# Optimization experiments

Measured on AMD Instinct MI355X. Metric: run time of the kernel, lower is better.

Reference implementation:

```python
import jax
import jax.numpy as jnp
import numpy as np
from jax import lax

DELTA = float(np.exp(-2.0))  # rule-creation density threshold


def codebook_lamb(x):
    """Online growing RBF prototype codebook (ALMMo-style) for one layer.

    x: [N, M]. Returns lamb: [N] normalized density of each sample at its
    assigned rule. Faithful (corrected) semantics of Layer.__call__:
      - SEN = squared L2 norm per sample (over feature dim)
      - global mean / mean squared norm over the batch
      - sequential per-sample: if max RBF density over existing rules < exp(-2),
        append a new rule (prototype=c=x, SENc=||x||^2, support=1);
        else update rule_star. Note the source's `support[rule_star] = +1`
        assigns 1, so the running mean update degenerates to c[rule_star]=x,
        SENc[rule_star]=||x||^2 -- replicated here.
      - distances use the (never-updated) prototypes; bandwidth stau uses c.
    """
    N, M = x.shape
    SENx = jnp.sum(x * x, axis=-1)                      # [N]
    gmean = jnp.mean(x, axis=0)                         # [M]
    base = jnp.mean(SENx) - jnp.sum(gmean * gmean)      # SENgmean - SEN(gmean)
    R = N                                               # worst case: one rule/sample

    protos0 = jnp.zeros((R, M), x.dtype)
    pn20 = jnp.zeros((R,), x.dtype)                     # ||proto_r||^2 (carried)
    c0 = jnp.zeros((R, M), x.dtype)
    cn20 = jnp.zeros((R,), x.dtype)                     # ||c_r||^2 (carried)
    SENc0 = jnp.zeros((R,), x.dtype)
    count0 = jnp.int32(0)

    ridx = jnp.arange(R)

    def step(carry, inp):
        protos, pn2, c, cn2, SENc, count = carry
        xi, sxi = inp                                   # [M], scalar
        valid = ridx < count
        stau = (base + SENc - cn2) * 0.5                # [R]
        dist = sxi + pn2 - 2.0 * (protos @ xi)          # [R] ||xi - proto_r||^2
        dens = jnp.where(valid, jnp.exp(-dist / stau), -jnp.inf)
        idx = jnp.argmax(dens)
        vmax = dens[idx]
        new = (count == 0) | (vmax < DELTA)
        slot = jnp.where(new, count, idx)
        # both branches set c/SENc at slot to xi/sxi (support resets to 1)
        c = c.at[slot].set(xi)
        cn2 = cn2.at[slot].set(sxi)
        SENc = SENc.at[slot].set(sxi)
        # only a new rule writes a prototype (OOB scatter when count==R is dropped)
        protos = protos.at[count].set(jnp.where(new, xi, protos[count]))
        pn2 = pn2.at[count].set(jnp.where(new, sxi, pn2[count]))
        count = count + new.astype(count.dtype)
        return (protos, pn2, c, cn2, SENc, count), slot

    (protos, pn2, c, cn2, SENc, count), rules = lax.scan(
        step, (protos0, pn20, c0, cn20, SENc0, count0), (x, SENx)
    )

    # final densities of all samples under all (valid) rules: [R, N]
    stau = (base + SENc - cn2) * 0.5                    # [R]
    dist = SENx[None, :] + pn2[:, None] - 2.0 * (protos @ x.T)
    dens = jnp.where((ridx < count)[:, None], jnp.exp(-dist / stau[:, None]), 0.0)
    dens_xn = dens[rules, jnp.arange(N)]                # density at assigned rule
    lamb = dens_xn / jnp.sum(dens, axis=0)              # normalize over rules
    return lamb


def setup_inputs() -> dict:
    key = jax.random.key(0)
    k = jax.random.split(key, 5)
    N, D_IN, D_H, D_OUT = 2048, 2048, 2048, 1024
    s0 = 1.0 / np.sqrt(D_IN)
    s1 = 1.0 / np.sqrt(D_H)
    return {
        "x": jax.random.normal(k[0], (N, D_IN), jnp.float32),
        "W0": jax.random.normal(k[1], (D_H, D_IN), jnp.float32) * s0,
        "b0": jax.random.normal(k[2], (D_H,), jnp.float32) * s0,
        "W1": jax.random.normal(k[3], (D_OUT, D_H), jnp.float32) * s1,
        "b1": jax.random.normal(k[4], (D_OUT,), jnp.float32) * s1,
    }


def reference(x, W0, b0, W1, b1):
    lambs = []
    h = x
    for W, b in ((W0, b0), (W1, b1)):
        lambs.append(codebook_lamb(h))          # per-layer codebook on layer input
        h = jax.nn.sigmoid(h @ W.T + b)         # torch.nn.Linear + sigmoid
    return h, jnp.stack(lambs)                  # ([N, d_out], [n_layers, N])
```

## Files before the change

kernel.cpp:

```cpp
#include <hip/hip_runtime.h>
#include <cstdint>
#include <cstddef>


#define DELTA_F 0.13533528323661270f
#define MBYTE (1u << 20)

typedef __bf16 bf16;
typedef bf16 bf16x8 __attribute__((ext_vector_type(8)));
typedef bf16 bf16x4 __attribute__((ext_vector_type(4)));
typedef float f32x4 __attribute__((ext_vector_type(4)));

typedef __attribute__((address_space(1))) void as1_void;
typedef __attribute__((address_space(3))) void as3_void;

__device__ __forceinline__ void gload16(const bf16* g, bf16* l) {
  __builtin_amdgcn_global_load_lds((as1_void*)g, (as3_void*)l, 16, 0, 0);
}

__device__ __forceinline__ float wave_reduce(float s) {
  for (int o = 32; o > 0; o >>= 1) s += __shfl_down(s, o, 64);
  return s;
}

template <bool IS_L0>
__global__ __launch_bounds__(512, 4) void gemm_fused(
    const bf16* __restrict__ A, float* __restrict__ Dens,
    bf16* __restrict__ Hb, float* __restrict__ Fo,
    const float* __restrict__ bias, const float* __restrict__ SENin,
    const float* __restrict__ ninv_p, float* __restrict__ S,
    int* __restrict__ e, float* __restrict__ SENhOut,
    float* __restrict__ colsumH, float* __restrict__ diagD,
    int* __restrict__ cnt, float* __restrict__ scalOut,
    float* __restrict__ lambOut, int nblocks) {
  __shared__ __align__(16) char smem[32768];
  __shared__ int s_last;
  const int tid = threadIdx.x;
  const int wave = tid >> 6, lane = tid & 63;
  const int quad = lane >> 4, l16 = lane & 15;
  const int kg = wave & 1, wm = (wave >> 1) & 1, wn = (wave >> 2) & 1;
  const int m0 = blockIdx.y * 128, n0 = blockIdx.x * 128;
  const int waveM = wm * 64, waveN = wn * 64;
  const bool isGram = (n0 < 2048);
  const int sr8 = lane >> 3, slot = lane & 7;
  const int gk = (slot ^ sr8) * 8;
  const bf16* aSrc = A + (size_t)(m0 + wave * 16 + sr8) * 2048 + gk;
  const bf16* bSrc = A + (size_t)(n0 + wave * 16 + sr8) * 2048 + gk;
  char* const aDst = smem + wave * 2048;
  char* const bDst = smem + 16384 + wave * 2048;
  const int swz = ((kg * 4 + quad) ^ (l16 & 7)) * 16;
  const int aOff = (waveM + l16) * 128 + swz;
  const int bOff = 16384 + (waveN + l16) * 128 + swz;

  f32x4 acc[4][4] = {};
  for (int k0 = 0; k0 < 2048; k0 += 64) {
    gload16(aSrc + k0, (bf16*)aDst);
    gload16(aSrc + 8 * 2048 + k0, (bf16*)(aDst + 1024));
    gload16(bSrc + k0, (bf16*)bDst);
    gload16(bSrc + 8 * 2048 + k0, (bf16*)(bDst + 1024));
    __syncthreads();
    bf16x8 af[4], bfr[4];
#pragma unroll
    for (int i = 0; i < 4; ++i) af[i] = *(const bf16x8*)(smem + aOff + i * 2048);
#pragma unroll
    for (int j = 0; j < 4; ++j) bfr[j] = *(const bf16x8*)(smem + bOff + j * 2048);
#pragma unroll
    for (int i = 0; i < 4; ++i)
#pragma unroll
      for (int j = 0; j < 4; ++j)
        acc[i][j] = __builtin_amdgcn_mfma_f32_16x16x32_bf16(af[i], bfr[j], acc[i][j], 0, 0, 0);
    __syncthreads();
  }

  const float ninv = ninv_p[0];
  float colp[4] = {0.f, 0.f, 0.f, 0.f};
  char* const ex = smem + (wn * 2 + wm) * 8192;
#pragma unroll
  for (int round = 0; round < 2; ++round) {
    __syncthreads();
    if (kg == 1) {
#pragma unroll
      for (int ii = 0; ii < 2; ++ii)
#pragma unroll
        for (int j = 0; j < 4; ++j)
          *(f32x4*)(ex + (ii * 4 + j) * 1024 + lane * 16) = acc[round * 2 + ii][j];
    }
    __syncthreads();
    if (kg == 0) {
#pragma unroll
      for (int ii = 0; ii < 2; ++ii) {
        const int i = round * 2 + ii;
        const int rbase = m0 + waveM + i * 16 + quad * 4;
        if (isGram) {
          const f32x4 si4 = *(const f32x4*)(SENin + rbase);
          float rp[4] = {0.f, 0.f, 0.f, 0.f};
          int er = 0;
#pragma unroll
          for (int j = 0; j < 4; ++j) {
            f32x4 v = acc[i][j] + *(const f32x4*)(ex + (ii * 4 + j) * 1024 + lane * 16);
            const int col = n0 + waveN + j * 16 + l16;
            const float sj = SENin[col];
#pragma unroll
            for (int r = 0; r < 4; ++r) {
              const float dens = __expf((si4[r] + sj - 2.0f * v[r]) * ninv);
              Dens[(size_t)(rbase + r) * 2048 + col] = dens;
              rp[r] += dens;
              if (col < rbase + r && dens >= DELTA_F) er |= (1 << r);
              if (col == rbase + r) atomicExch(diagD + col, dens);
            }
          }
#pragma unroll
          for (int r = 0; r < 4; ++r) {
            float rv = rp[r];
            rv += __shfl_xor(rv, 1, 64); rv += __shfl_xor(rv, 2, 64);
            rv += __shfl_xor(rv, 4, 64); rv += __shfl_xor(rv, 8, 64);
            if (l16 == 0) atomicAdd(S + rbase + r, rv);
          }
          er |= __shfl_xor(er, 1, 64); er |= __shfl_xor(er, 2, 64);
          er |= __shfl_xor(er, 4, 64); er |= __shfl_xor(er, 8, 64);
          if (l16 == 0 && er) {
#pragma unroll
            for (int r = 0; r < 4; ++r)
              if ((er >> r) & 1) atomicOr(e + rbase + r, 1);
          }
        } else {
          float rn[4] = {0.f, 0.f, 0.f, 0.f};
#pragma unroll
          for (int j = 0; j < 4; ++j) {
            f32x4 v = acc[i][j] + *(const f32x4*)(ex + (ii * 4 + j) * 1024 + lane * 16);
            const int c2 = n0 - 2048 + waveN + j * 16 + l16;
            const float bv = bias[c2];
#pragma unroll
            for (int r = 0; r < 4; ++r) {
              const float hv = 1.0f / (1.0f + __expf(-(v[r] + bv)));
              if (IS_L0) {
                Hb[(size_t)(rbase + r) * 2048 + c2] = (bf16)hv;
                rn[r] += hv * hv;
                colp[j] += hv;
              } else {
                Fo[(size_t)(rbase + r) * 1024 + c2] = hv;
              }
            }
          }
          if (IS_L0) {
#pragma unroll
            for (int r = 0; r < 4; ++r) {
              float rv = rn[r];
              rv += __shfl_xor(rv, 1, 64); rv += __shfl_xor(rv, 2, 64);
              rv += __shfl_xor(rv, 4, 64); rv += __shfl_xor(rv, 8, 64);
              if (l16 == 0) atomicAdd(SENhOut + rbase + r, rv);
            }
          }
        }
      }
    }
  }
  if (IS_L0 && !isGram && kg == 0) {
#pragma unroll
    for (int j = 0; j < 4; ++j) {
      float cv = colp[j];
      cv += __shfl_xor(cv, 16, 64);
      cv += __shfl_xor(cv, 32, 64);
      if (lane < 16) atomicAdd(colsumH + (n0 - 2048 + waveN + j * 16 + lane), cv);
    }
  }

  __syncthreads();
  if (tid == 0) s_last = (atomicAdd(cnt, 1) == nblocks - 1);
  __syncthreads();
  if (!s_last) return;

  char* s_flag = smem;
  short* s_as = (short*)(smem + 2048);
  short* s_list = (short*)(smem + 6144);
  short* s_re = (short*)(smem + 10240);
  int* scan_ = (int*)(smem + 14336);
  float* rbest = (float*)(smem + 16384);
  int* rbj = (int*)(smem + 18432);
  float* r1 = (float*)(smem + 20480);
  float* r2 = (float*)(smem + 22528);
  int* sT = (int*)(smem + 24576);
  int* sReN = (int*)(smem + 24580);

  if (IS_L0) {
    float ssen = 0.f, sg2 = 0.f;
    for (int i = tid; i < 2048; i += 512) ssen += atomicAdd(SENhOut + i, 0.f);
    for (int c = tid; c < 2048; c += 512) {
      const float gm = atomicAdd(colsumH + c, 0.f) * (1.f / 2048.f);
      sg2 += gm * gm;
    }
    r1[tid] = ssen; r2[tid] = sg2;
    __syncthreads();
    for (int s = 256; s; s >>= 1) {
      if (tid < s) { r1[tid] += r1[tid + s]; r2[tid] += r2[tid + s]; }
      __syncthreads();
    }
    if (tid == 0) {
      const float stau = 0.5f * (r1[0] * (1.f / 2048.f) - r2[0]);
      scalOut[4] = stau;
      scalOut[5] = -1.f / stau;
    }
    __syncthreads();
  }

  int cntl = 0;
#pragma unroll
  for (int k = 0; k < 4; ++k) {
    const int i = tid * 4 + k;
    const int ei = atomicOr(e + i, 0);
    s_flag[i] = (ei == 0);
    if (ei == 0) s_as[i] = (short)i;
    cntl += (ei != 0);
  }
  scan_[tid] = cntl;
  if (tid == 0) sReN[0] = 0;
  __syncthreads();
  for (int off = 1; off < 512; off <<= 1) {
    const int v = scan_[tid];
    const int add = (tid >= off) ? scan_[tid - off] : 0;
    __syncthreads();
    scan_[tid] = v + add;
    __syncthreads();
  }
  int pos = scan_[tid] - cntl;
#pragma unroll
  for (int k = 0; k < 4; ++k) {
    const int i = tid * 4 + k;
    if (!s_flag[i]) s_list[pos++] = (short)i;
  }
  if (tid == 511) sT[0] = scan_[511];
  __syncthreads();
  const int T = sT[0];
  if (T > 0) __threadfence();
  for (int t = 0; t < T; ++t) {
    const int i = s_list[t];
    const float* di = Dens + (size_t)i * 2048;
    float best = -1.0f;
    int bestj = 0x7fffffff;
    for (int j = tid; j < i; j += 512) {
      if (s_flag[j]) {
        const float d = di[j];
        if (d > best || (d == best && j < bestj)) { best = d; bestj = j; }
      }
    }
    rbest[tid] = best; rbj[tid] = bestj;
    __syncthreads();
    if (tid == 0) {
      float b = -1.0f;
      int bj = 0x7fffffff;
      for (int k = 0; k < 512; ++k)
        if (rbest[k] > b || (rbest[k] == b && rbj[k] < bj)) { b = rbest[k]; bj = rbj[k]; }
      if (b < DELTA_F) { s_flag[i] = 1; s_as[i] = (short)i; }
      else { s_as[i] = (short)bj; s_re[sReN[0]++] = (short)i; }
    }
    __syncthreads();
  }
  const int reN = sReN[0];

#pragma unroll
  for (int k = 0; k < 4; ++k) {
    const int n = k * 512 + tid;
    const int aa = s_as[n];
    const float num = (aa == n) ? atomicAdd(diagD + n, 0.f)
                                : Dens[(size_t)n * 2048 + aa];
    float denom = atomicAdd(S + n, 0.f);
    for (int t = 0; t < reN; ++t) denom -= Dens[(size_t)n * 2048 + s_re[t]];
    lambOut[n] = num / denom;
  }
}

__global__ void f2b_all(const float* __restrict__ x, const float* __restrict__ W0,
                        const float* __restrict__ W1, bf16* __restrict__ xb,
                        bf16* __restrict__ wb0, bf16* __restrict__ wb1,
                        float* __restrict__ SENx, float* __restrict__ bins,
                        int* __restrict__ cntF, float* __restrict__ scal) {
  const int b = blockIdx.x, tid = threadIdx.x;
  const int wave = tid >> 6, lane = tid & 63;
  __shared__ float ws[8][4];
  __shared__ float red1[256], red2[256];
  __shared__ int s_last;
  if (b < 256) {
    const int r0 = b * 8;
    f32x4 c0 = {0.f, 0.f, 0.f, 0.f}, c1 = {0.f, 0.f, 0.f, 0.f};
    for (int r = 0; r < 8; ++r) {
      const float* src = x + (size_t)(r0 + r) * 2048;
      bf16* dst = xb + (size_t)(r0 + r) * 2048;
      f32x4 v0 = *(const f32x4*)(src + tid * 4);
      f32x4 v1 = *(const f32x4*)(src + 1024 + tid * 4);
      bf16x4 o0, o1;
      o0.x = (bf16)v0.x; o0.y = (bf16)v0.y; o0.z = (bf16)v0.z; o0.w = (bf16)v0.w;
      o1.x = (bf16)v1.x; o1.y = (bf16)v1.y; o1.z = (bf16)v1.z; o1.w = (bf16)v1.w;
      *(bf16x4*)(dst + tid * 4) = o0;
      *(bf16x4*)(dst + 1024 + tid * 4) = o1;
      c0 += v0; c1 += v1;
      float rn = v0.x * v0.x + v0.y * v0.y + v0.z * v0.z + v0.w * v0.w +
                 v1.x * v1.x + v1.y * v1.y + v1.z * v1.z + v1.w * v1.w;
      rn = wave_reduce(rn);
      if (lane == 0) ws[r][wave] = rn;
    }
    __syncthreads();
    if (tid < 8)
      atomicExch(SENx + r0 + tid, ws[tid][0] + ws[tid][1] + ws[tid][2] + ws[tid][3]);
    float* bin = bins + (size_t)(b & 15) * 2048;
    atomicAdd(bin + tid * 4 + 0, c0.x); atomicAdd(bin + tid * 4 + 1, c0.y);
    atomicAdd(bin + tid * 4 + 2, c0.z); atomicAdd(bin + tid * 4 + 3, c0.w);
    atomicAdd(bin + 1024 + tid * 4 + 0, c1.x); atomicAdd(bin + 1024 + tid * 4 + 1, c1.y);
    atomicAdd(bin + 1024 + tid * 4 + 2, c1.z); atomicAdd(bin + 1024 + tid * 4 + 3, c1.w);
  } else if (b < 512) {
    const size_t base = (size_t)(b - 256) * 16384;
    for (int c = tid * 4; c < 16384; c += 1024) {
      f32x4 v = *(const f32x4*)(W0 + base + c);
      bf16x4 o;
      o.x = (bf16)v.x; o.y = (bf16)v.y; o.z = (bf16)v.z; o.w = (bf16)v.w;
      *(bf16x4*)(wb0 + base + c) = o;
    }
  } else {
    const size_t base = (size_t)(b - 512) * 16384;
    for (int c = tid * 4; c < 16384; c += 1024) {
      f32x4 v = *(const f32x4*)(W1 + base + c);
      bf16x4 o;
      o.x = (bf16)v.x; o.y = (bf16)v.y; o.z = (bf16)v.z; o.w = (bf16)v.w;
      *(bf16x4*)(wb1 + base + c) = o;
    }
  }

  __syncthreads();
  if (tid == 0) s_last = (atomicAdd(cntF, 1) == 639);
  __syncthreads();
  if (!s_last) return;
  float ssen = 0.f;
  for (int i = tid; i < 2048; i += 256) ssen += atomicAdd(SENx + i, 0.f);
  float sg2 = 0.f;
  for (int c = tid; c < 2048; c += 256) {
    float cs = 0.f;
#pragma unroll
    for (int p = 0; p < 16; ++p) cs += atomicAdd(bins + (size_t)p * 2048 + c, 0.f);
    const float gm = cs * (1.f / 2048.f);
    sg2 += gm * gm;
  }
  red1[tid] = ssen; red2[tid] = sg2;
  __syncthreads();
  for (int s = 128; s; s >>= 1) {
    if (tid < s) { red1[tid] += red1[tid + s]; red2[tid] += red2[tid + s]; }
    __syncthreads();
  }
  if (tid == 0) {
    const float stau = 0.5f * (red1[0] * (1.f / 2048.f) - red2[0]);
    scal[0] = stau;
    scal[1] = -1.f / stau;
  }
}

extern "C" void kernel_launch(void* const* d_in, const int* in_sizes, int n_in,
                              void* d_out, int out_size, void* d_ws, size_t ws_size,
                              hipStream_t stream) {
  const float* x = (const float*)d_in[0];
  const float* W0 = (const float*)d_in[1];
  const float* b0 = (const float*)d_in[2];
  const float* W1 = (const float*)d_in[3];
  const float* b1 = (const float*)d_in[4];
  float* out = (float*)d_out;

  char* w = (char*)d_ws;
  bf16* xb = (bf16*)(w);
  bf16* wb0 = (bf16*)(w + 8 * MBYTE);
  bf16* hb = (bf16*)(w + 16 * MBYTE);
  bf16* wb1 = (bf16*)(w + 24 * MBYTE);
  float* Dens = (float*)(w + 28 * MBYTE);
  float* SENx = (float*)(w + 44 * MBYTE);
  float* scal = SENx + 2048;
  float* zre = scal + 16;
  float* bins = zre;
  float* SENh = bins + 16 * 2048;
  float* colsumH = SENh + 2048;
  float* S0 = colsumH + 2048;
  float* S1 = S0 + 2048;
  float* diagD0 = S1 + 2048;
  float* diagD1 = diagD0 + 2048;
  int* e0 = (int*)(diagD1 + 2048);
  int* e1 = e0 + 2048;
  int* cntF = e1 + 2048;
  int* cnt0 = cntF + 1;
  int* cnt1 = cnt0 + 1;
  const size_t zwords = 16 * 2048 + 8 * 2048 + 16;

  float* lamb0 = out + (size_t)2048 * 1024;
  float* lamb1 = lamb0 + 2048;

  hipMemsetAsync(zre, 0, zwords * 4, stream);
  f2b_all<<<640, 256, 0, stream>>>(x, W0, W1, xb, wb0, wb1, SENx, bins, cntF, scal);
  gemm_fused<true><<<dim3(32, 16), 512, 0, stream>>>(
      xb, Dens, hb, nullptr, b0, SENx, scal + 1, S0, e0, SENh, colsumH,
      diagD0, cnt0, scal, lamb0, 512);
  gemm_fused<false><<<dim3(24, 16), 512, 0, stream>>>(
      hb, Dens, nullptr, out, b1, SENh, scal + 5, S1, e1, nullptr, nullptr,
      diagD1, cnt1, nullptr, lamb1, 384);
}
```

Measured before the change: 203.4 us.

## Move layer-0 rule decision into extra block of layer-1 GEMM kernel

The serial layer-0 rule-assignment and lambda pass no longer runs in the last finishing block of the layer-0 GEMM. It now runs in an extra block column of the layer-1 kernel, so it overlaps with the layer-1 GEMM. That extra block also computes the layer-1 bandwidth scalar and publishes it through a global flag, which the Gram tiles spin-wait on. Layer 1 gets its own density buffer so the two passes do not collide. The spin-wait could deadlock if the extra block is not scheduled, and it adds contention.

Result: faster. 195.2 us (-4.0%).

```diff
diff --git a/kernel.cpp b/kernel.cpp
--- a/kernel.cpp
+++ b/kernel.cpp
@@ -21,6 +21,85 @@
 __device__ __forceinline__ float wave_reduce(float s) {
   for (int o = 32; o > 0; o >>= 1) s += __shfl_down(s, o, 64);
   return s;
+}
+
+template <bool SAME>
+__device__ void run_decide_lamb(char* smem, int* e, float* Dens, float* S,
+                                float* diagD, float* lambOut) {
+  char* s_flag = smem;
+  short* s_as = (short*)(smem + 2048);
+  short* s_list = (short*)(smem + 6144);
+  short* s_re = (short*)(smem + 10240);
+  int* scan_ = (int*)(smem + 14336);
+  float* rbest = (float*)(smem + 16384);
+  int* rbj = (int*)(smem + 18432);
+  int* sT = (int*)(smem + 24576);
+  int* sReN = (int*)(smem + 24580);
+  const int tid = threadIdx.x;
+  int cntl = 0;
+#pragma unroll
+  for (int k = 0; k < 4; ++k) {
+    const int i = tid * 4 + k;
+    const int ei = SAME ? atomicOr(e + i, 0) : e[i];
+    s_flag[i] = (ei == 0);
+    if (ei == 0) s_as[i] = (short)i;
+    cntl += (ei != 0);
+  }
+  scan_[tid] = cntl;
+  if (tid == 0) sReN[0] = 0;
+  __syncthreads();
+  for (int off = 1; off < 512; off <<= 1) {
+    const int v = scan_[tid];
+    const int add = (tid >= off) ? scan_[tid - off] : 0;
+    __syncthreads();
+    scan_[tid] = v + add;
+    __syncthreads();
+  }
+  int pos = scan_[tid] - cntl;
+#pragma unroll
+  for (int k = 0; k < 4; ++k) {
+    const int i = tid * 4 + k;
+    if (!s_flag[i]) s_list[pos++] = (short)i;
+  }
+  if (tid == 511) sT[0] = scan_[511];
+  __syncthreads();
+  const int T = sT[0];
+  if (SAME && T > 0) __threadfence();
+  for (int t = 0; t < T; ++t) {
+    const int i = s_list[t];
+    const float* di = Dens + (size_t)i * 2048;
+    float best = -1.0f;
+    int bestj = 0x7fffffff;
+    for (int j = tid; j < i; j += 512) {
+      if (s_flag[j]) {
+        const float d = di[j];
+        if (d > best || (d == best && j < bestj)) { best = d; bestj = j; }
+      }
+    }
+    rbest[tid] = best; rbj[tid] = bestj;
+    __syncthreads();
+    if (tid == 0) {
+      float b = -1.0f;
+      int bj = 0x7fffffff;
+      for (int k = 0; k < 512; ++k)
+        if (rbest[k] > b || (rbest[k] == b && rbj[k] < bj)) { b = rbest[k]; bj = rbj[k]; }
+      if (b < DELTA_F) { s_flag[i] = 1; s_as[i] = (short)i; }
+      else { s_as[i] = (short)bj; s_re[sReN[0]++] = (short)i; }
+    }
+    __syncthreads();
+  }
+  const int reN = sReN[0];
+#pragma unroll
+  for (int k = 0; k < 4; ++k) {
+    const int n = k * 512 + tid;
+    const int aa = s_as[n];
+    const float num = (aa == n)
+        ? (SAME ? atomicAdd(diagD + n, 0.f) : diagD[n])
+        : Dens[(size_t)n * 2048 + aa];
+    float denom = SAME ? atomicAdd(S + n, 0.f) : S[n];
+    for (int t = 0; t < reN; ++t) denom -= Dens[(size_t)n * 2048 + s_re[t]];
+    lambOut[n] = num / denom;
+  }
 }
 
 template <bool IS_L0>
@@ -31,11 +110,40 @@
     const float* __restrict__ ninv_p, float* __restrict__ S,
     int* __restrict__ e, float* __restrict__ SENhOut,
     float* __restrict__ colsumH, float* __restrict__ diagD,
-    int* __restrict__ cnt, float* __restrict__ scalOut,
-    float* __restrict__ lambOut, int nblocks) {
+    int* __restrict__ cnt, int nblocks, float* __restrict__ lambOut,
+    int* __restrict__ flagN, const float* __restrict__ SENh_r,
+    const float* __restrict__ colsumH_r, int* __restrict__ e0,
+    float* __restrict__ S0, float* __restrict__ diag0,
+    float* __restrict__ Dens0, float* __restrict__ lamb0) {
   __shared__ __align__(16) char smem[32768];
   __shared__ int s_last;
   const int tid = threadIdx.x;
+
+  if (!IS_L0 && blockIdx.x == 24) {
+    if (blockIdx.y != 0) return;
+    float* r1 = (float*)(smem + 20480);
+    float* r2 = (float*)(smem + 22528);
+    float ssen = 0.f, sg2 = 0.f;
+    for (int i = tid; i < 2048; i += 512) ssen += SENh_r[i];
+    for (int c = tid; c < 2048; c += 512) {
+      const float gm = colsumH_r[c] * (1.f / 2048.f);
+      sg2 += gm * gm;
+    }
+    r1[tid] = ssen; r2[tid] = sg2;
+    __syncthreads();
+    for (int s = 256; s; s >>= 1) {
+      if (tid < s) { r1[tid] += r1[tid + s]; r2[tid] += r2[tid + s]; }
+      __syncthreads();
+    }
+    if (tid == 0) {
+      const float stau = 0.5f * (r1[0] * (1.f / 2048.f) - r2[0]);
+      atomicExch(flagN, __float_as_int(-1.f / stau));
+    }
+    __syncthreads();
+    run_decide_lamb<false>(smem, e0, Dens0, S0, diag0, lamb0);
+    return;
+  }
+
   const int wave = tid >> 6, lane = tid & 63;
   const int quad = lane >> 4, l16 = lane & 15;
   const int kg = wave & 1, wm = (wave >> 1) & 1, wn = (wave >> 2) & 1;
@@ -72,7 +180,16 @@
     __syncthreads();
   }
 
-  const float ninv = ninv_p[0];
+  float ninv = 0.f;
+  if (isGram) {
+    if (IS_L0) ninv = ninv_p[0];
+    else {
+      int fi;
+      while ((fi = atomicOr(flagN, 0)) == 0) {}
+      ninv = __int_as_float(fi);
+    }
+  }
+
   float colp[4] = {0.f, 0.f, 0.f, 0.f};
   char* const ex = smem + (wn * 2 + wm) * 8192;
 #pragma unroll
@@ -165,108 +282,13 @@
     }
   }
 
+  if (IS_L0) return;
+
   __syncthreads();
   if (tid == 0) s_last = (atomicAdd(cnt, 1) == nblocks - 1);
   __syncthreads();
   if (!s_last) return;
-
-  char* s_flag = smem;
-  short* s_as = (short*)(smem + 2048);
-  short* s_list = (short*)(smem + 6144);
-  short* s_re = (short*)(smem + 10240);
-  int* scan_ = (int*)(smem + 14336);
-  float* rbest = (float*)(smem + 16384);
-  int* rbj = (int*)(smem + 18432);
-  float* r1 = (float*)(smem + 20480);
-  float* r2 = (float*)(smem + 22528);
-  int* sT = (int*)(smem + 24576);
-  int* sReN = (int*)(smem + 24580);
-
-  if (IS_L0) {
-    float ssen = 0.f, sg2 = 0.f;
-    for (int i = tid; i < 2048; i += 512) ssen += atomicAdd(SENhOut + i, 0.f);
-    for (int c = tid; c < 2048; c += 512) {
-      const float gm = atomicAdd(colsumH + c, 0.f) * (1.f / 2048.f);
-      sg2 += gm * gm;
-    }
-    r1[tid] = ssen; r2[tid] = sg2;
-    __syncthreads();
-    for (int s = 256; s; s >>= 1) {
-      if (tid < s) { r1[tid] += r1[tid + s]; r2[tid] += r2[tid + s]; }
-      __syncthreads();
-    }
-    if (tid == 0) {
-      const float stau = 0.5f * (r1[0] * (1.f / 2048.f) - r2[0]);
-      scalOut[4] = stau;
-      scalOut[5] = -1.f / stau;
-    }
-    __syncthreads();
-  }
-
-  int cntl = 0;
-#pragma unroll
-  for (int k = 0; k < 4; ++k) {
-    const int i = tid * 4 + k;
-    const int ei = atomicOr(e + i, 0);
-    s_flag[i] = (ei == 0);
-    if (ei == 0) s_as[i] = (short)i;
-    cntl += (ei != 0);
-  }
-  scan_[tid] = cntl;
-  if (tid == 0) sReN[0] = 0;
-  __syncthreads();
-  for (int off = 1; off < 512; off <<= 1) {
-    const int v = scan_[tid];
-    const int add = (tid >= off) ? scan_[tid - off] : 0;
-    __syncthreads();
-    scan_[tid] = v + add;
-    __syncthreads();
-  }
-  int pos = scan_[tid] - cntl;
-#pragma unroll
-  for (int k = 0; k < 4; ++k) {
-    const int i = tid * 4 + k;
-    if (!s_flag[i]) s_list[pos++] = (short)i;
-  }
-  if (tid == 511) sT[0] = scan_[511];
-  __syncthreads();
-  const int T = sT[0];
-  if (T > 0) __threadfence();
-  for (int t = 0; t < T; ++t) {
-    const int i = s_list[t];
-    const float* di = Dens + (size_t)i * 2048;
-    float best = -1.0f;
-    int bestj = 0x7fffffff;
-    for (int j = tid; j < i; j += 512) {
-      if (s_flag[j]) {
-        const float d = di[j];
-        if (d > best || (d == best && j < bestj)) { best = d; bestj = j; }
-      }
-    }
-    rbest[tid] = best; rbj[tid] = bestj;
-    __syncthreads();
-    if (tid == 0) {
-      float b = -1.0f;
-      int bj = 0x7fffffff;
-      for (int k = 0; k < 512; ++k)
-        if (rbest[k] > b || (rbest[k] == b && rbj[k] < bj)) { b = rbest[k]; bj = rbj[k]; }
-      if (b < DELTA_F) { s_flag[i] = 1; s_as[i] = (short)i; }
-      else { s_as[i] = (short)bj; s_re[sReN[0]++] = (short)i; }
-    }
-    __syncthreads();
-  }
-  const int reN = sReN[0];
-
-#pragma unroll
-  for (int k = 0; k < 4; ++k) {
-    const int n = k * 512 + tid;
-    const int aa = s_as[n];
-    const float num = (aa == n) ? atomicAdd(diagD + n, 0.f)
-                                : Dens[(size_t)n * 2048 + aa];
-    float denom = atomicAdd(S + n, 0.f);
-    for (int t = 0; t < reN; ++t) denom -= Dens[(size_t)n * 2048 + s_re[t]];
-    lambOut[n] = num / denom;
-  }
+  run_decide_lamb<true>(smem, e, Dens, S, diagD, lambOut);
 }
 
 __global__ void f2b_all(const float* __restrict__ x, const float* __restrict__ W0,
@@ -366,7 +388,8 @@
   bf16* wb0 = (bf16*)(w + 8 * MBYTE);
   bf16* hb = (bf16*)(w + 16 * MBYTE);
   bf16* wb1 = (bf16*)(w + 24 * MBYTE);
-  float* Dens = (float*)(w + 28 * MBYTE);
+  float* Dens0 = (float*)(w + 28 * MBYTE);
+  float* Dens1 = (float*)(w);
   float* SENx = (float*)(w + 44 * MBYTE);
   float* scal = SENx + 2048;
   float* zre = scal + 16;
@@ -380,8 +403,8 @@
   int* e0 = (int*)(diagD1 + 2048);
   int* e1 = e0 + 2048;
   int* cntF = e1 + 2048;
-  int* cnt0 = cntF + 1;
-  int* cnt1 = cnt0 + 1;
+  int* cnt1 = cntF + 1;
+  int* flagN = cnt1 + 1;
   const size_t zwords = 16 * 2048 + 8 * 2048 + 16;
 
   float* lamb0 = out + (size_t)2048 * 1024;
@@ -390,9 +413,11 @@
   hipMemsetAsync(zre, 0, zwords * 4, stream);
   f2b_all<<<640, 256, 0, stream>>>(x, W0, W1, xb, wb0, wb1, SENx, bins, cntF, scal);
   gemm_fused<true><<<dim3(32, 16), 512, 0, stream>>>(
-      xb, Dens, hb, nullptr, b0, SENx, scal + 1, S0, e0, SENh, colsumH,
-      diagD0, cnt0, scal, lamb0, 512);
-  gemm_fused<false><<<dim3(24, 16), 512, 0, stream>>>(
-      hb, Dens, nullptr, out, b1, SENh, scal + 5, S1, e1, nullptr, nullptr,
-      diagD1, cnt1, nullptr, lamb1, 384);
-}
+      xb, Dens0, hb, nullptr, b0, SENx, scal + 1, S0, e0, SENh, colsumH,
+      diagD0, nullptr, 0, nullptr,
+      nullptr, nullptr, nullptr, nullptr, nullptr, nullptr, nullptr, nullptr);
+  gemm_fused<false><<<dim3(25, 16), 512, 0, stream>>>(
+      hb, Dens1, nullptr, out, b1, SENh, nullptr, S1, e1, nullptr, nullptr,
+      diagD1, cnt1, 384, lamb1,
+      flagN, SENh, colsumH, e0, S0, diagD0, Dens0, lamb0);
+}
```
